# Optimization experiments

Hardware: AMD Instinct MI355X
Metric: run time of the kernel (lower is better)

## Reference

```python
import jax, jax.numpy as jnp
import numpy as np

C_IN = 3; IMG = 256; LAT = 256; K = 1024; L = 4
ENC = [128, 256, 512]; DEC = [512, 256, 128]


def conv2d(x, w, b, stride, pad):
    # x: NCHW, w: OIHW
    y = jax.lax.conv_general_dilated(x, w, (stride, stride), [(pad, pad), (pad, pad)],
                                     dimension_numbers=('NCHW', 'OIHW', 'NCHW'))
    return y + b[None, :, None, None]


def convT(x, w, b):
    # stride-2 transposed conv, kernel 4, 'SAME' -> doubles H,W. w: HWIO
    y = jax.lax.conv_transpose(x, w, (2, 2), 'SAME',
                               dimension_numbers=('NCHW', 'HWIO', 'NCHW'))
    return y + b[None, :, None, None]


def setup_inputs() -> dict:
    key = jax.random.key(0)
    ks = iter(jax.random.split(key, 32))
    def w(shape, fan_in):
        return jax.random.normal(next(ks), shape, jnp.float32) / np.float32(np.sqrt(fan_in))
    inp = {'x': jax.random.normal(next(ks), (8, C_IN, IMG, IMG), jnp.float32)}
    cin = C_IN
    for i, co in enumerate(ENC):
        inp[f'enc_w{i}'] = w((co, cin, 4, 4), cin * 16)
        inp[f'enc_b{i}'] = jnp.zeros((co,), jnp.float32)
        cin = co
    inp['proj_w'] = w((LAT, ENC[-1], 1, 1), ENC[-1])
    inp['proj_b'] = jnp.zeros((LAT,), jnp.float32)
    cin = LAT
    for i, co in enumerate(DEC):
        inp[f'dec_w{i}'] = w((4, 4, cin, co), cin * 16)
        inp[f'dec_b{i}'] = jnp.zeros((co,), jnp.float32)
        cin = co
    inp['out_w'] = w((C_IN, DEC[-1], 3, 3), DEC[-1] * 9)
    inp['out_b'] = jnp.zeros((C_IN,), jnp.float32)
    # per-level codebooks, uniform(-1/K, 1/K) as in the torch init
    inp['emb'] = jax.random.uniform(next(ks), (L, K, LAT), jnp.float32, -1.0 / K, 1.0 / K)
    return inp


def reference(x, enc_w0, enc_b0, enc_w1, enc_b1, enc_w2, enc_b2,
              proj_w, proj_b, dec_w0, dec_b0, dec_w1, dec_b1, dec_w2, dec_b2,
              out_w, out_b, emb):
    # encoder: three stride-2 convs + ReLU
    h = x
    for w_, b_ in ((enc_w0, enc_b0), (enc_w1, enc_b1), (enc_w2, enc_b2)):
        h = jax.nn.relu(conv2d(h, w_, b_, 2, 1))
    z = conv2d(h, proj_w, proj_b, 1, 0)  # [B, LAT, 32, 32]

    # residual quantization over L levels
    B, C, H, W = z.shape
    r = z
    z_q = jnp.zeros_like(z)
    residuals, codes = [], []
    for l in range(L):
        E = emb[l]                                   # [K, C]
        rf = r.transpose(0, 2, 3, 1).reshape(-1, C)  # [B*H*W, C]
        # squared euclidean distance (argmin equal to cdist argmin)
        d2 = (jnp.sum(rf * rf, axis=1, keepdims=True)
              - 2.0 * (rf @ E.T)
              + jnp.sum(E * E, axis=1))
        idx = jnp.argmin(d2, axis=1)                 # [B*H*W]
        e = E[idx].reshape(B, H, W, C).transpose(0, 3, 1, 2)
        residuals.append(r)
        codes.append(idx.reshape(B, H, W))
        z_q = z_q + e
        r = r - e

    # straight-through estimator
    z_q_st = z + jax.lax.stop_gradient(z_q - z)

    # decoder: three stride-2 transposed convs + ReLU, then 3x3 output conv
    d = z_q_st
    for w_, b_ in ((dec_w0, dec_b0), (dec_w1, dec_b1), (dec_w2, dec_b2)):
        d = jax.nn.relu(convT(d, w_, b_))
    recon = conv2d(d, out_w, out_b, 1, 1)  # [B, 3, 256, 256] == img_size, no interp
    return recon, z, z_q, jnp.stack(residuals), jnp.stack(codes)
```

## Files before the change

kernel.cpp:

```cpp
#include <hip/hip_runtime.h>
#include <hip/hip_bf16.h>
#include <cstdint>

#define BATCH 8
#define LATC 256
#define NCODE 1024
#define NLVL 4

typedef __attribute__((ext_vector_type(8))) short bf16x8v;
typedef __attribute__((ext_vector_type(4))) float f32x4v;

__device__ __forceinline__ unsigned short f2b(float f) {
  __hip_bfloat16 h = __float2bfloat16(f);
  return *reinterpret_cast<unsigned short*>(&h);
}

__device__ __forceinline__ void gl_lds16(const void* gptr, unsigned lds_byte_off) {
  unsigned m0v = __builtin_amdgcn_readfirstlane(lds_byte_off);
  asm volatile("s_mov_b32 m0, %0\n"
               "global_load_lds_dwordx4 %1, off\n" ::"s"(m0v), "v"(gptr)
               : "memory");
}

template <int CIN, int COUT, int HIN, int CI_CHUNK, int CO_TILE, int CI_SPLIT>
__global__ __launch_bounds__(256) void conv_enc2(
    const float* __restrict__ in, const float* __restrict__ w,
    const float* __restrict__ bias, float* __restrict__ out) {
  constexpr int WIN = HIN;
  constexpr int HOUT = HIN / 2, WOUT = WIN / 2;
  constexpr int PT1 = HOUT / 16;
  constexpr int NEL = CI_CHUNK * 34 * 34;
  constexpr int WUNITS = CI_CHUNK * CO_TILE * 4;
  constexpr int CIPS = CIN / CI_SPLIT;

  __shared__ float T[CI_CHUNK][34][40];
  __shared__ float4 Wsh[CI_CHUNK][CO_TILE][4];

  const int tid = threadIdx.x;
  const int lane = tid & 63;
  const int wv = __builtin_amdgcn_readfirstlane(tid >> 6);
  const int cog = lane >> 5;
  const int pxi = lane & 31;
  const int m = pxi >> 2;
  const int ox4 = pxi & 3;
  const int co_loc0 = (wv * 2 + cog) * 8;

  const int bx = blockIdx.x;
  const int n = bx / (PT1 * PT1);
  const int pt = bx % (PT1 * PT1);
  const int oh0 = (pt / PT1) * 16, ow0 = (pt % PT1) * 16;
  const int hbase = 2 * oh0 - 1, wbase = 2 * ow0 - 1;
  const int co_blk = blockIdx.y * CO_TILE;
  const int split = (CI_SPLIT > 1) ? blockIdx.z : 0;
  const int ci_base = split * CIPS;

  float acc[2][4][2][4];
#pragma unroll
  for (int cl = 0; cl < 2; ++cl)
#pragma unroll
    for (int j = 0; j < 4; ++j) {
      float b = (CI_SPLIT == 1 || split == 0) ? bias[co_blk + co_loc0 + cl * 4 + j] : 0.f;
#pragma unroll
      for (int dy = 0; dy < 2; ++dy)
#pragma unroll
        for (int dx = 0; dx < 4; ++dx) acc[cl][j][dy][dx] = b;
    }

  for (int ch = ci_base; ch < ci_base + CIPS; ch += CI_CHUNK) {
    for (int u = tid; u < NEL; u += 256) {
      int cir = u / 1156;
      int rem = u - cir * 1156;
      int r = rem / 34, c = rem - r * 34;
      int hi = hbase + r, wi = wbase + c;
      float v = 0.f;
      if ((unsigned)hi < (unsigned)HIN && (unsigned)wi < (unsigned)WIN)
        v = in[((long long)(n * CIN + ch + cir) * HIN + hi) * WIN + wi];
      T[cir][r][(((r >> 2) & 1) << 2) + c] = v;
    }
    for (int u = tid; u < WUNITS; u += 256) {
      int k4 = u & 3;
      int rem = u >> 2;
      int co = rem % CO_TILE, ci = rem / CO_TILE;
      Wsh[ci][co][k4] =
          *(const float4*)&w[((long long)(co_blk + co) * CIN + ch + ci) * 16 + k4 * 4];
    }
    __syncthreads();
#pragma unroll
    for (int cir = 0; cir < CI_CHUNK; ++cir) {
      float xv[6][10];
#pragma unroll
      for (int roff = 0; roff < 6; ++roff) {
        int row = 4 * m + roff;
        const float* base = &T[cir][row][(((row >> 2) & 1) << 2) + 8 * ox4];
        float4 qa = *(const float4*)base;
        float4 qb = *(const float4*)(base + 4);
        float4 qc = *(const float4*)(base + 8);
        xv[roff][0] = qa.x; xv[roff][1] = qa.y; xv[roff][2] = qa.z; xv[roff][3] = qa.w;
        xv[roff][4] = qb.x; xv[roff][5] = qb.y; xv[roff][6] = qb.z; xv[roff][7] = qb.w;
        xv[roff][8] = qc.x; xv[roff][9] = qc.y;
      }
#pragma unroll
      for (int cl = 0; cl < 2; ++cl)
#pragma unroll
        for (int j = 0; j < 4; ++j) {
          int co_l = co_loc0 + cl * 4 + j;
#pragma unroll
          for (int kh = 0; kh < 4; ++kh) {
            float4 wq = Wsh[cir][co_l][kh];
            float wt0 = wq.x, wt1 = wq.y, wt2 = wq.z, wt3 = wq.w;
#pragma unroll
            for (int dy = 0; dy < 2; ++dy) {
              int r = 2 * dy + kh;
#pragma unroll
              for (int dx = 0; dx < 4; ++dx) {
                acc[cl][j][dy][dx] = fmaf(xv[r][2 * dx + 0], wt0, acc[cl][j][dy][dx]);
                acc[cl][j][dy][dx] = fmaf(xv[r][2 * dx + 1], wt1, acc[cl][j][dy][dx]);
                acc[cl][j][dy][dx] = fmaf(xv[r][2 * dx + 2], wt2, acc[cl][j][dy][dx]);
                acc[cl][j][dy][dx] = fmaf(xv[r][2 * dx + 3], wt3, acc[cl][j][dy][dx]);
              }
            }
          }
        }
    }
    __syncthreads();
  }
  const long long psz = (long long)BATCH * COUT * HOUT * WOUT;
  float* __restrict__ ob_ptr = out + (CI_SPLIT > 1 ? (long long)split * psz : 0LL);
#pragma unroll
  for (int cl = 0; cl < 2; ++cl)
#pragma unroll
    for (int j = 0; j < 4; ++j) {
      int co = co_blk + co_loc0 + cl * 4 + j;
#pragma unroll
      for (int dy = 0; dy < 2; ++dy) {
        int oh = oh0 + 2 * m + dy, ow = ow0 + 4 * ox4;
        float4 v;
#pragma unroll
        for (int dx = 0; dx < 4; ++dx) {
          float t = acc[cl][j][dy][dx];
          if (CI_SPLIT == 1) t = fmaxf(t, 0.f);
          ((float*)&v)[dx] = t;
        }
        *reinterpret_cast<float4*>(
            &ob_ptr[((long long)(n * COUT + co) * HOUT + oh) * WOUT + ow]) = v;
      }
    }
}

template <int S, bool RELU>
__global__ __launch_bounds__(256) void fuse_sum(const float* __restrict__ p,
                                                float* __restrict__ out, long long n4) {
  long long i = (long long)blockIdx.x * 256 + threadIdx.x;
  long long stride = (long long)gridDim.x * 256;
  long long N = n4 * 4;
  for (; i < n4; i += stride) {
    float4 a = *(const float4*)&p[i * 4];
#pragma unroll
    for (int s = 1; s < S; ++s) {
      float4 b = *(const float4*)&p[(long long)s * N + i * 4];
      a.x += b.x; a.y += b.y; a.z += b.z; a.w += b.w;
    }
    if (RELU) {
      a.x = fmaxf(a.x, 0.f); a.y = fmaxf(a.y, 0.f);
      a.z = fmaxf(a.z, 0.f); a.w = fmaxf(a.w, 0.f);
    }
    *(float4*)&out[i * 4] = a;
  }
}

__global__ __launch_bounds__(256) void wtrans(const float* __restrict__ pw,
                                              float* __restrict__ pwT) {
  int gid = blockIdx.x * 256 + threadIdx.x;
  if (gid >= 512 * 256) return;
  int ci = gid >> 8, co = gid & 255;
  pwT[gid] = pw[co * 512 + ci];
}

template <int CI_SPLIT>
__global__ __launch_bounds__(256) void conv1x1_v2(
    const float* __restrict__ in, const float* __restrict__ pwT,
    const float* __restrict__ bias, float* __restrict__ out) {
  constexpr int CIPS = 512 / CI_SPLIT;
  __shared__ float Tx[16][128];
  const int tid = threadIdx.x;
  const int lane = tid & 63;
  const int wv = __builtin_amdgcn_readfirstlane(tid >> 6);
  const int p0 = lane * 2;
  const int bx = blockIdx.x;
  const int n = bx >> 3, pxb = bx & 7;
  const int px_base = pxb * 128;
  const int co_base = blockIdx.y * 64 + wv * 16;
  const int split = (CI_SPLIT > 1) ? blockIdx.z : 0;
  const int ci0 = split * CIPS;

  float acc[4][4][2];
#pragma unroll
  for (int cl = 0; cl < 4; ++cl)
#pragma unroll
    for (int j = 0; j < 4; ++j) {
      float b = (CI_SPLIT == 1 || split == 0) ? bias[co_base + cl * 4 + j] : 0.f;
      acc[cl][j][0] = b; acc[cl][j][1] = b;
    }

  for (int ch = ci0; ch < ci0 + CIPS; ch += 16) {
    for (int u = tid; u < 2048; u += 256) {
      int cir = u >> 7, p = u & 127;
      Tx[cir][p] = in[(long long)(n * 512 + ch + cir) * 1024 + px_base + p];
    }
    __syncthreads();
#pragma unroll
    for (int cir = 0; cir < 16; ++cir) {
      float2 xv = *reinterpret_cast<const float2*>(&Tx[cir][p0]);
#pragma unroll
      for (int cl = 0; cl < 4; ++cl) {
        const float* __restrict__ wp = pwT + (ch + cir) * 256 + co_base + cl * 4;
#pragma unroll
        for (int j = 0; j < 4; ++j) {
          float wt = wp[j];
          acc[cl][j][0] = fmaf(xv.x, wt, acc[cl][j][0]);
          acc[cl][j][1] = fmaf(xv.y, wt, acc[cl][j][1]);
        }
      }
    }
    __syncthreads();
  }
  const long long psz = (long long)BATCH * 256 * 1024;
  float* __restrict__ ob = out + (CI_SPLIT > 1 ? (long long)split * psz : 0LL);
#pragma unroll
  for (int cl = 0; cl < 4; ++cl)
#pragma unroll
    for (int j = 0; j < 4; ++j) {
      int co = co_base + cl * 4 + j;
      *reinterpret_cast<float2*>(&ob[(long long)(n * 256 + co) * 1024 + px_base + p0]) =
          make_float2(acc[cl][j][0], acc[cl][j][1]);
    }
}

__global__ __launch_bounds__(256) void emb_norms(
    const float* __restrict__ emb, float* __restrict__ en) {
  int k = blockIdx.x * blockDim.x + threadIdx.x;
  if (k >= NLVL * NCODE) return;
  const float* __restrict__ e = emb + (long long)k * LATC;
  float s = 0.f;
  for (int c = 0; c < LATC; ++c) s = fmaf(e[c], e[c], s);
  en[k] = s;
}

#define RQ_P 32
#define RQ_CT 32
#define RQ_RS 260

__global__ __launch_bounds__(256) void rq_kernel2(
    const float* __restrict__ z, const float* __restrict__ emb,
    const float* __restrict__ en, float* __restrict__ zq_out,
    float* __restrict__ resid_out, float* __restrict__ codes_out) {
  __shared__ float e_sh[RQ_CT * RQ_RS];
  __shared__ float r_sh[RQ_P * RQ_RS];
  __shared__ float sum_sh[RQ_P];
  __shared__ int code_sh[RQ_P];
  const int tid = threadIdx.x;
  const int blk = blockIdx.x;
  const int n = (blk * RQ_P) >> 10;
  const int hw0 = (blk * RQ_P) & 1023;
  const long long zb = ((long long)n * LATC) * 1024 + hw0;

  for (int it = 0; it < 32; ++it) {
    int u = it * 256 + tid;
    int c = u >> 5, pix = u & 31;
    float v = z[zb + (long long)c * 1024 + pix];
    r_sh[pix * RQ_RS + c] = v;
    resid_out[((long long)n * LATC + c) * 1024 + hw0 + pix] = v;
  }
  __syncthreads();

  const int code_l = tid & 31;
  const int pixoff = tid >> 5;
  const int upix = tid >> 3;
  const int ucg = tid & 7;

  for (int l = 0; l < NLVL; ++l) {
    {
      float s = 0.f;
#pragma unroll
      for (int it = 0; it < 8; ++it) {
        int c4 = ucg + it * 8;
        float4 r4 = *(const float4*)&r_sh[upix * RQ_RS + c4 * 4];
        s += r4.x * r4.x + r4.y * r4.y + r4.z * r4.z + r4.w * r4.w;
      }
      s += __shfl_xor(s, 1); s += __shfl_xor(s, 2); s += __shfl_xor(s, 4);
      if (ucg == 0) sum_sh[upix] = s;
    }
    __syncthreads();
    const float* __restrict__ E = emb + (long long)l * NCODE * LATC;
    const float* __restrict__ enl = en + l * NCODE;
    float best[4]; int bidx[4];
#pragma unroll
    for (int g = 0; g < 4; ++g) { best[g] = 3.4e38f; bidx[g] = 0; }
    for (int tile = 0; tile < NCODE / RQ_CT; ++tile) {
      const float* __restrict__ Et = E + (long long)tile * RQ_CT * LATC;
      for (int it = 0; it < 32; ++it) {
        int u = it * 256 + tid;
        int cc = u >> 8, ch = u & 255;
        e_sh[cc * RQ_RS + ch] = Et[cc * LATC + ch];
      }
      __syncthreads();
      float acc[4] = {0.f, 0.f, 0.f, 0.f};
      for (int c4 = 0; c4 < 64; ++c4) {
        float4 e4 = *(const float4*)&e_sh[code_l * RQ_RS + c4 * 4];
#pragma unroll
        for (int g = 0; g < 4; ++g) {
          float4 r4 = *(const float4*)&r_sh[(g * 8 + pixoff) * RQ_RS + c4 * 4];
          acc[g] = fmaf(r4.x, e4.x, acc[g]);
          acc[g] = fmaf(r4.y, e4.y, acc[g]);
          acc[g] = fmaf(r4.z, e4.z, acc[g]);
          acc[g] = fmaf(r4.w, e4.w, acc[g]);
        }
      }
      int code = tile * RQ_CT + code_l;
      float ek2 = enl[code];
#pragma unroll
      for (int g = 0; g < 4; ++g) {
        float d2 = (sum_sh[g * 8 + pixoff] - 2.f * acc[g]) + ek2;
        if (d2 < best[g]) { best[g] = d2; bidx[g] = code; }
      }
      __syncthreads();
    }
#pragma unroll
    for (int g = 0; g < 4; ++g) {
      float bd = best[g]; int bi = bidx[g];
#pragma unroll
      for (int m = 1; m < 32; m <<= 1) {
        float od = __shfl_xor(bd, m);
        int oi = __shfl_xor(bi, m);
        if (od < bd || (od == bd && oi < bi)) { bd = od; bi = oi; }
      }
      if (code_l == 0) {
        int pix = g * 8 + pixoff;
        code_sh[pix] = bi;
        codes_out[(long long)(l * BATCH + n) * 1024 + hw0 + pix] = (float)bi;
      }
    }
    __syncthreads();
    {
      int sel = code_sh[upix];
      const float* __restrict__ esel = E + (long long)sel * LATC;
#pragma unroll
      for (int it = 0; it < 8; ++it) {
        int c4 = ucg + it * 8;
        float4 r4 = *(const float4*)&r_sh[upix * RQ_RS + c4 * 4];
        float4 e4 = *(const float4*)&esel[c4 * 4];
        r4.x -= e4.x; r4.y -= e4.y; r4.z -= e4.z; r4.w -= e4.w;
        *(float4*)&r_sh[upix * RQ_RS + c4 * 4] = r4;
        if (l < NLVL - 1) {
          long long rb = ((long long)((l + 1) * BATCH + n) * LATC + c4 * 4) * 1024 + hw0 + upix;
          resid_out[rb] = r4.x;
          resid_out[rb + 1024] = r4.y;
          resid_out[rb + 2048] = r4.z;
          resid_out[rb + 3072] = r4.w;
        }
      }
    }
    __syncthreads();
  }
  for (int it = 0; it < 32; ++it) {
    int u = it * 256 + tid;
    int c = u >> 5, pix = u & 31;
    float zv = z[zb + (long long)c * 1024 + pix];
    zq_out[zb + (long long)c * 1024 + pix] = zv - r_sh[pix * RQ_RS + c];
  }
}

__global__ __launch_bounds__(256) void to_nhwc_s1(const float* __restrict__ zq,
                                                  unsigned short* __restrict__ o) {
  __shared__ float tsh[32][33];
  int bx = blockIdx.x;
  int ct = bx & 7, y = (bx >> 3) & 31, n = bx >> 8;
  int tid = threadIdx.x;
  int x = tid & 31, cl = tid >> 5;
#pragma unroll
  for (int it = 0; it < 4; ++it) {
    int ci = it * 8 + cl;
    tsh[ci][x] = zq[((long long)(n * 256 + ct * 32 + ci) * 32 + y) * 32 + x];
  }
  __syncthreads();
  int ci = tid & 31, xg = tid >> 5;
#pragma unroll
  for (int it = 0; it < 4; ++it) {
    int xw = it * 8 + xg;
    o[(((long long)n * 34 + y + 1) * 34 + xw + 1) * 256 + ct * 32 + ci] = f2b(tsh[ci][xw]);
  }
}

__global__ __launch_bounds__(256) void wprep_k(const float* __restrict__ w,
                                               unsigned short* __restrict__ o,
                                               int CINc, int COUTc) {
  long long total = 16LL * CINc * COUTc;
  long long gid = (long long)blockIdx.x * 256 + threadIdx.x;
  if (gid >= total) return;
  int ci32 = (int)(gid & 31); long long t = gid >> 5;
  int co = (int)(t % COUTc); t /= COUTc;
  int tap = (int)(t & 3); t >>= 2;
  int nch = CINc / 32;
  int ch = (int)(t % nch); int phase = (int)(t / nch);
  int py = phase >> 1, px = phase & 1;
  int ky = py + 2 * (tap >> 1), kx = px + 2 * (tap & 1);
  int ci = ch * 32 + ci32;
  float v = w[(((long long)ky * 4 + kx) * CINc + ci) * COUTc + co];
  o[gid] = f2b(v);
}

template <int CIN, int COUT, int TH, int TW, int Hi, int Wi, bool OUT_NCHW>
__global__ __launch_bounds__(256) void convt2(
    const unsigned short* __restrict__ xin, const unsigned short* __restrict__ wprep,
    const float* __restrict__ bias, unsigned short* __restrict__ outp) {
  constexpr int TWP = TW + 2, ROWS = TH + 2;
  constexpr int Hp = Hi + 2, Wp = Wi + 2;
  constexpr int NCH = CIN / 32;
  constexpr int XUNITS = ROWS * TWP;
  constexpr int XPAD = ((XUNITS + 255) / 256) * 256;
  constexpr int WBASE = 4 * XPAD;
  __shared__ unsigned short lds[(4 * XPAD + 4 * 256) * 8];

  const int tid = threadIdx.x;
  const int wv = tid >> 6, lane = tid & 63;
  const int l15 = lane & 15, seg = lane >> 4;

  constexpr int SW = Wi / TW, SH = Hi / TH;
  const int bx = blockIdx.x;
  const int n = bx / (SH * SW);
  const int srem = bx % (SH * SW);
  const int i0 = (srem / SW) * TH, j0 = (srem % SW) * TW;
  const int cob0 = blockIdx.y * 64;
  const int phase = blockIdx.z;
  const int pyp = phase >> 1, pxp = phase & 1;

  const unsigned short* xsrc = xin + (long long)n * Hp * Wp * CIN;

  f32x4v acc[4][4];
  if (!OUT_NCHW) {
#pragma unroll
    for (int b = 0; b < 4; ++b) {
      float bv = bias[cob0 + b * 16 + l15];
      f32x4v v = {bv, bv, bv, bv};
#pragma unroll
      for (int a = 0; a < 4; ++a) acc[a][b] = v;
    }
  } else {
#pragma unroll
    for (int a = 0; a < 4; ++a) {
      f32x4v v;
#pragma unroll
      for (int q = 0; q < 4; ++q) v[q] = bias[cob0 + a * 16 + seg * 4 + q];
#pragma unroll
      for (int b = 0; b < 4; ++b) acc[a][b] = v;
    }
  }

  for (int ch = 0; ch < NCH; ++ch) {
    __syncthreads();
#pragma unroll
    for (int sg = 0; sg < 4; ++sg) {
#pragma unroll
      for (int it = 0; it < XPAD / 256; ++it) {
        int u = it * 256 + tid;
        int us = u < XUNITS ? u : XUNITS - 1;
        int row = us / TWP, col = us % TWP;
        const unsigned short* g =
            xsrc + ((long long)(i0 + row) * Wp + (j0 + col)) * CIN + ch * 32 + sg * 8;
        gl_lds16(g, (unsigned)(unsigned long long)(const void*)&lds[(sg * XPAD + u) * 8]);
      }
    }
    {
      const unsigned short* wb = wprep + ((long long)phase * NCH + ch) * 4 * COUT * 32;
      int tap = tid >> 6, co = tid & 63;
#pragma unroll
      for (int sg = 0; sg < 4; ++sg) {
        const unsigned short* g = wb + ((long long)tap * COUT + cob0 + co) * 32 + sg * 8;
        gl_lds16(g, (unsigned)(unsigned long long)(const void*)&lds[(WBASE + sg * 256 + tid) * 8]);
      }
    }
    asm volatile("s_waitcnt vmcnt(0)" ::: "memory");
    __syncthreads();
#pragma unroll
    for (int t = 0; t < 4; ++t) {
      int oy = (t >> 1) - 1 + pyp, ox = (t & 1) - 1 + pxp;
      bf16x8v xf[4], wf[4];
#pragma unroll
      for (int i = 0; i < 4; ++i) {
        int p = wv * 64 + i * 16 + l15;
        int r = p / TW, c = p % TW;
        int xrow = r + oy + 1, xcol = c + ox + 1;
        xf[i] = *(const bf16x8v*)&lds[(seg * XPAD + xrow * TWP + xcol) * 8];
        wf[i] = *(const bf16x8v*)&lds[(WBASE + seg * 256 + t * 64 + i * 16 + l15) * 8];
      }
#pragma unroll
      for (int a = 0; a < 4; ++a)
#pragma unroll
        for (int b = 0; b < 4; ++b) {
          if (OUT_NCHW)
            acc[a][b] = __builtin_amdgcn_mfma_f32_16x16x32_bf16(wf[a], xf[b], acc[a][b], 0, 0, 0);
          else
            acc[a][b] = __builtin_amdgcn_mfma_f32_16x16x32_bf16(xf[a], wf[b], acc[a][b], 0, 0, 0);
        }
    }
  }

  if (!OUT_NCHW) {
    constexpr int Wpo = 2 * Wi + 2;
    long long ob_n = (long long)n * (2 * Hi + 2) * Wpo * COUT;
#pragma unroll
    for (int a = 0; a < 4; ++a)
#pragma unroll
      for (int q = 0; q < 4; ++q) {
        int p = wv * 64 + a * 16 + seg * 4 + q;
        int r = p / TW, c = p % TW;
        int yo = 2 * (i0 + r) + pyp + 1, xo = 2 * (j0 + c) + pxp + 1;
        long long ob = ob_n + ((long long)yo * Wpo + xo) * COUT + cob0;
#pragma unroll
        for (int b = 0; b < 4; ++b) {
          float v = fmaxf(acc[a][b][q], 0.f);
          outp[ob + b * 16 + l15] = f2b(v);
        }
      }
  } else {
    constexpr int Ho = 2 * Hi, Wo = 2 * Wi;
#pragma unroll
    for (int a = 0; a < 4; ++a)
#pragma unroll
      for (int q = 0; q < 4; ++q) {
        int co = cob0 + a * 16 + seg * 4 + q;
#pragma unroll
        for (int b = 0; b < 4; ++b) {
          int p = wv * 64 + b * 16 + l15;
          int r = p / TW, c = p % TW;
          int yo = 2 * (i0 + r) + pyp, xo = 2 * (j0 + c) + pxp;
          float v = fmaxf(acc[a][b][q], 0.f);
          outp[((long long)(n * COUT + co) * Ho + yo) * Wo + xo] = f2b(v);
        }
      }
  }
}

__global__ __launch_bounds__(256) void conv3x3_v2(
    const __hip_bfloat16* __restrict__ in, const float* __restrict__ w,
    const float* __restrict__ bias, float* __restrict__ out) {
  constexpr int H = 256, W = 256, CIN = 128;
  __shared__ float Wsh[3 * CIN * 9];
  __shared__ float T[4][34][35];

  const int tid = threadIdx.x;
  for (int u = tid; u < 3 * CIN * 9; u += 256) Wsh[u] = w[u];

  const int bx = blockIdx.x;
  const int n = bx >> 6;
  const int t8 = bx & 63;
  const int y0 = (t8 >> 3) * 32, x0 = (t8 & 7) * 32;
  const int ty = (tid >> 4) * 2;
  const int tx = (tid & 15) * 2;

  float acc[3][2][2];
#pragma unroll
  for (int co = 0; co < 3; ++co) {
    float b = bias[co];
    acc[co][0][0] = b; acc[co][0][1] = b; acc[co][1][0] = b; acc[co][1][1] = b;
  }

  for (int ch = 0; ch < CIN; ch += 4) {
    __syncthreads();
    for (int u = tid; u < 4 * 34 * 34; u += 256) {
      int ci = u / (34 * 34);
      int rem = u % (34 * 34);
      int r = rem / 34, c = rem % 34;
      int yy = y0 + r - 1, xx = x0 + c - 1;
      float v = 0.f;
      if ((unsigned)yy < (unsigned)H && (unsigned)xx < (unsigned)W)
        v = __bfloat162float(in[((long long)(n * CIN + ch + ci) * H + yy) * W + xx]);
      T[ci][r][c] = v;
    }
    __syncthreads();
#pragma unroll
    for (int ci = 0; ci < 4; ++ci) {
      float xv[4][4];
#pragma unroll
      for (int r = 0; r < 4; ++r)
#pragma unroll
        for (int c = 0; c < 4; ++c) xv[r][c] = T[ci][ty + r][tx + c];
#pragma unroll
      for (int co = 0; co < 3; ++co) {
        const float* __restrict__ wp = &Wsh[(co * CIN + ch + ci) * 9];
#pragma unroll
        for (int kh = 0; kh < 3; ++kh)
#pragma unroll
          for (int kw = 0; kw < 3; ++kw) {
            float wt = wp[kh * 3 + kw];
            acc[co][0][0] = fmaf(xv[kh][kw], wt, acc[co][0][0]);
            acc[co][0][1] = fmaf(xv[kh][kw + 1], wt, acc[co][0][1]);
            acc[co][1][0] = fmaf(xv[kh + 1][kw], wt, acc[co][1][0]);
            acc[co][1][1] = fmaf(xv[kh + 1][kw + 1], wt, acc[co][1][1]);
          }
      }
    }
  }
#pragma unroll
  for (int co = 0; co < 3; ++co)
#pragma unroll
    for (int dy = 0; dy < 2; ++dy) {
      long long ob = ((long long)(n * 3 + co) * H + y0 + ty + dy) * W + x0 + tx;
      *reinterpret_cast<float2*>(&out[ob]) = make_float2(acc[co][dy][0], acc[co][dy][1]);
    }
}

extern "C" void kernel_launch(void* const* d_in, const int* in_sizes, int n_in,
                              void* d_out, int out_size, void* d_ws, size_t ws_size,
                              hipStream_t stream) {
  const float* x   = (const float*)d_in[0];
  const float* ew0 = (const float*)d_in[1];  const float* eb0 = (const float*)d_in[2];
  const float* ew1 = (const float*)d_in[3];  const float* eb1 = (const float*)d_in[4];
  const float* ew2 = (const float*)d_in[5];  const float* eb2 = (const float*)d_in[6];
  const float* pw  = (const float*)d_in[7];  const float* pb  = (const float*)d_in[8];
  const float* dw0 = (const float*)d_in[9];  const float* db0 = (const float*)d_in[10];
  const float* dw1 = (const float*)d_in[11]; const float* db1 = (const float*)d_in[12];
  const float* dw2 = (const float*)d_in[13]; const float* db2 = (const float*)d_in[14];
  const float* ow  = (const float*)d_in[15]; const float* ob  = (const float*)d_in[16];
  const float* emb = (const float*)d_in[17];

  float* out   = (float*)d_out;
  float* recon = out;
  float* z     = out + 1572864;
  float* zq    = out + 3670016;
  float* resid = out + 5767168;
  float* codes = out + 14155776;

  char* ws = (char*)d_ws;
  dim3 blk(256);
  auto g = [](long long tot) { return dim3((unsigned)((tot + 255) / 256)); };

  const size_t OFF_S1IN  = 0ULL;
  const size_t OFF_S1OUT = 4734976ULL;
  const size_t OFF_WP1   = 40419328ULL;
  const size_t OFF_WP2   = 44613632ULL;
  const size_t OFF_P     = 67108864ULL;
  const size_t OFF_E2    = 134217728ULL;
  const size_t OFF_PWT   = 150994944ULL;
  const size_t OFF_DD2   = 0ULL;
  const size_t OFF_S2OUT = 134217728ULL;
  const size_t OFF_WP3   = 203440128ULL;
  const size_t OFF_EN    = 204488704ULL;
  const size_t WS_NEED   = 204505088ULL;

  if (ws_size < WS_NEED) return;

  float* e0  = (float*)(ws);
  float* p2  = (float*)(ws + OFF_P);
  float* e1  = (float*)(ws);
  float* p3  = (float*)(ws + OFF_P);
  float* e2  = (float*)(ws + OFF_E2);
  float* q1  = (float*)(ws + OFF_P);
  float* en  = (float*)(ws + OFF_EN);
  float* pwT = (float*)(ws + OFF_PWT);
  unsigned short* s1in  = (unsigned short*)(ws + OFF_S1IN);
  unsigned short* s1out = (unsigned short*)(ws + OFF_S1OUT);
  unsigned short* s2out = (unsigned short*)(ws + OFF_S2OUT);
  unsigned short* dd2   = (unsigned short*)(ws + OFF_DD2);
  unsigned short* wp1   = (unsigned short*)(ws + OFF_WP1);
  unsigned short* wp2   = (unsigned short*)(ws + OFF_WP2);
  unsigned short* wp3   = (unsigned short*)(ws + OFF_WP3);

  emb_norms<<<g(4096), blk, 0, stream>>>(emb, en);

  conv_enc2<3, 128, 256, 3, 64, 1><<<dim3(512, 2, 1), blk, 0, stream>>>(x, ew0, eb0, e0);
  conv_enc2<128, 256, 128, 4, 64, 4><<<dim3(128, 4, 4), blk, 0, stream>>>(e0, ew1, eb1, p2);
  fuse_sum<4, true><<<dim3(4096), blk, 0, stream>>>(p2, e1, 8388608 / 4);
  conv_enc2<256, 512, 64, 4, 64, 4><<<dim3(32, 8, 4), blk, 0, stream>>>(e1, ew2, eb2, p3);
  fuse_sum<4, true><<<dim3(2048), blk, 0, stream>>>(p3, e2, 4194304 / 4);
  wtrans<<<g(512 * 256), blk, 0, stream>>>(pw, pwT);
  conv1x1_v2<4><<<dim3(64, 4, 4), blk, 0, stream>>>(e2, pwT, pb, q1);
  fuse_sum<4, false><<<dim3(1024), blk, 0, stream>>>(q1, z, 2097152 / 4);

  rq_kernel2<<<dim3(256), blk, 0, stream>>>(z, emb, en, zq, resid, codes);

  hipMemsetAsync(ws + OFF_S1IN, 0, 4734976ULL, stream);
  hipMemsetAsync(ws + OFF_S1OUT, 0, 35684352ULL, stream);
  hipMemsetAsync(ws + OFF_S2OUT, 0, 69222400ULL, stream);
  to_nhwc_s1<<<dim3(2048), blk, 0, stream>>>(zq, s1in);
  wprep_k<<<g(16LL * 256 * 512), blk, 0, stream>>>(dw0, wp1, 256, 512);
  wprep_k<<<g(16LL * 512 * 256), blk, 0, stream>>>(dw1, wp2, 512, 256);
  wprep_k<<<g(16LL * 256 * 128), blk, 0, stream>>>(dw2, wp3, 256, 128);

  convt2<256, 512, 8, 32, 32, 32, false>
      <<<dim3(32, 8, 4), dim3(256), 0, stream>>>(s1in, wp1, db0, s1out);
  convt2<512, 256, 4, 64, 64, 64, false>
      <<<dim3(128, 4, 4), dim3(256), 0, stream>>>(s1out, wp2, db1, s2out);
  convt2<256, 128, 4, 64, 128, 128, true>
      <<<dim3(512, 2, 4), dim3(256), 0, stream>>>(s2out, wp3, db2, dd2);

  conv3x3_v2<<<dim3(512), blk, 0, stream>>>((const __hip_bfloat16*)dd2, ow, ob, recon);
}
```

Before: 2.777 ms.

## Restructure residual quantization with register-tiled 4x4 codes-by-pixels dot products

The RQ kernel now keeps the residual transposed in LDS (channel-major) and gives each thread a 4-code by 4-pixel register tile. Each wave owns a quarter of the codebook, and codebook rows are read directly from global memory instead of being staged through LDS tiles with per-tile barriers. A cross-wave argmin reduction through shared memory replaces the per-tile shuffle reduction. This aims to raise arithmetic intensity and remove barrier and LDS staging overhead, at the cost of strided uncached-looking global reads of the codebook and more registers.

```diff
diff --git a/kernel.cpp b/kernel.cpp
--- a/kernel.cpp
+++ b/kernel.cpp
@@ -246,35 +246,35 @@
   en[k] = s;
 }
 
-#define RQ_P 32
-#define RQ_CT 32
-#define RQ_RS 260
-
-__global__ __launch_bounds__(256) void rq_kernel2(
+__global__ __launch_bounds__(256) void rq_kernel3(
     const float* __restrict__ z, const float* __restrict__ emb,
     const float* __restrict__ en, float* __restrict__ zq_out,
     float* __restrict__ resid_out, float* __restrict__ codes_out) {
-  __shared__ float e_sh[RQ_CT * RQ_RS];
-  __shared__ float r_sh[RQ_P * RQ_RS];
-  __shared__ float sum_sh[RQ_P];
-  __shared__ int code_sh[RQ_P];
+  __shared__ float rT[256 * 32];
+  __shared__ float sum_sh[32];
+  __shared__ float red_d[4][32];
+  __shared__ int red_i[4][32];
+  __shared__ int code_sh[32];
+
   const int tid = threadIdx.x;
+  const int lane = tid & 63;
+  const int w = __builtin_amdgcn_readfirstlane(tid >> 6);
+  const int cs = lane & 7;
+  const int ps = lane >> 3;
   const int blk = blockIdx.x;
-  const int n = (blk * RQ_P) >> 10;
-  const int hw0 = (blk * RQ_P) & 1023;
+  const int n = (blk * 32) >> 10;
+  const int hw0 = (blk * 32) & 1023;
   const long long zb = ((long long)n * LATC) * 1024 + hw0;
 
   for (int it = 0; it < 32; ++it) {
     int u = it * 256 + tid;
     int c = u >> 5, pix = u & 31;
     float v = z[zb + (long long)c * 1024 + pix];
-    r_sh[pix * RQ_RS + c] = v;
+    rT[c * 32 + pix] = v;
     resid_out[((long long)n * LATC + c) * 1024 + hw0 + pix] = v;
   }
   __syncthreads();
 
-  const int code_l = tid & 31;
-  const int pixoff = tid >> 5;
   const int upix = tid >> 3;
   const int ucg = tid & 7;
 
@@ -284,79 +284,116 @@
 #pragma unroll
       for (int it = 0; it < 8; ++it) {
         int c4 = ucg + it * 8;
-        float4 r4 = *(const float4*)&r_sh[upix * RQ_RS + c4 * 4];
-        s += r4.x * r4.x + r4.y * r4.y + r4.z * r4.z + r4.w * r4.w;
+        float x = rT[(c4 * 4 + 0) * 32 + upix];
+        float y = rT[(c4 * 4 + 1) * 32 + upix];
+        float zz = rT[(c4 * 4 + 2) * 32 + upix];
+        float ww = rT[(c4 * 4 + 3) * 32 + upix];
+        s += x * x + y * y + zz * zz + ww * ww;
       }
       s += __shfl_xor(s, 1); s += __shfl_xor(s, 2); s += __shfl_xor(s, 4);
       if (ucg == 0) sum_sh[upix] = s;
     }
     __syncthreads();
+
     const float* __restrict__ E = emb + (long long)l * NCODE * LATC;
     const float* __restrict__ enl = en + l * NCODE;
-    float best[4]; int bidx[4];
-#pragma unroll
-    for (int g = 0; g < 4; ++g) { best[g] = 3.4e38f; bidx[g] = 0; }
-    for (int tile = 0; tile < NCODE / RQ_CT; ++tile) {
-      const float* __restrict__ Et = E + (long long)tile * RQ_CT * LATC;
-      for (int it = 0; it < 32; ++it) {
-        int u = it * 256 + tid;
-        int cc = u >> 8, ch = u & 255;
-        e_sh[cc * RQ_RS + ch] = Et[cc * LATC + ch];
-      }
-      __syncthreads();
-      float acc[4] = {0.f, 0.f, 0.f, 0.f};
+    float bd[4]; int bi[4];
+#pragma unroll
+    for (int i = 0; i < 4; ++i) { bd[i] = 3.4e38f; bi[i] = 0; }
+
+    for (int pass = 0; pass < 8; ++pass) {
+      const int cbase = w * 256 + pass * 32 + cs * 4;
+      float acc[4][4];
+#pragma unroll
+      for (int j = 0; j < 4; ++j)
+#pragma unroll
+        for (int i = 0; i < 4; ++i) acc[j][i] = 0.f;
+#pragma unroll 4
       for (int c4 = 0; c4 < 64; ++c4) {
-        float4 e4 = *(const float4*)&e_sh[code_l * RQ_RS + c4 * 4];
-#pragma unroll
-        for (int g = 0; g < 4; ++g) {
-          float4 r4 = *(const float4*)&r_sh[(g * 8 + pixoff) * RQ_RS + c4 * 4];
-          acc[g] = fmaf(r4.x, e4.x, acc[g]);
-          acc[g] = fmaf(r4.y, e4.y, acc[g]);
-          acc[g] = fmaf(r4.z, e4.z, acc[g]);
-          acc[g] = fmaf(r4.w, e4.w, acc[g]);
-        }
-      }
-      int code = tile * RQ_CT + code_l;
-      float ek2 = enl[code];
-#pragma unroll
-      for (int g = 0; g < 4; ++g) {
-        float d2 = (sum_sh[g * 8 + pixoff] - 2.f * acc[g]) + ek2;
-        if (d2 < best[g]) { best[g] = d2; bidx[g] = code; }
-      }
-      __syncthreads();
-    }
-#pragma unroll
-    for (int g = 0; g < 4; ++g) {
-      float bd = best[g]; int bi = bidx[g];
-#pragma unroll
-      for (int m = 1; m < 32; m <<= 1) {
-        float od = __shfl_xor(bd, m);
-        int oi = __shfl_xor(bi, m);
-        if (od < bd || (od == bd && oi < bi)) { bd = od; bi = oi; }
-      }
-      if (code_l == 0) {
-        int pix = g * 8 + pixoff;
-        code_sh[pix] = bi;
-        codes_out[(long long)(l * BATCH + n) * 1024 + hw0 + pix] = (float)bi;
-      }
-    }
-    __syncthreads();
+        float4 ee[4];
+#pragma unroll
+        for (int j = 0; j < 4; ++j)
+          ee[j] = *(const float4*)&E[(long long)(cbase + j) * LATC + c4 * 4];
+        float4 rr[4];
+#pragma unroll
+        for (int s = 0; s < 4; ++s)
+          rr[s] = *(const float4*)&rT[(c4 * 4 + s) * 32 + ps * 4];
+#pragma unroll
+        for (int j = 0; j < 4; ++j) {
+          acc[j][0] = fmaf(ee[j].x, rr[0].x, acc[j][0]);
+          acc[j][0] = fmaf(ee[j].y, rr[1].x, acc[j][0]);
+          acc[j][0] = fmaf(ee[j].z, rr[2].x, acc[j][0]);
+          acc[j][0] = fmaf(ee[j].w, rr[3].x, acc[j][0]);
+          acc[j][1] = fmaf(ee[j].x, rr[0].y, acc[j][1]);
+          acc[j][1] = fmaf(ee[j].y, rr[1].y, acc[j][1]);
+          acc[j][1] = fmaf(ee[j].z, rr[2].y, acc[j][1]);
+          acc[j][1] = fmaf(ee[j].w, rr[3].y, acc[j][1]);
+          acc[j][2] = fmaf(ee[j].x, rr[0].z, acc[j][2]);
+          acc[j][2] = fmaf(ee[j].y, rr[1].z, acc[j][2]);
+          acc[j][2] = fmaf(ee[j].z, rr[2].z, acc[j][2]);
+          acc[j][2] = fmaf(ee[j].w, rr[3].z, acc[j][2]);
+          acc[j][3] = fmaf(ee[j].x, rr[0].w, acc[j][3]);
+          acc[j][3] = fmaf(ee[j].y, rr[1].w, acc[j][3]);
+          acc[j][3] = fmaf(ee[j].z, rr[2].w, acc[j][3]);
+          acc[j][3] = fmaf(ee[j].w, rr[3].w, acc[j][3]);
+        }
+      }
+#pragma unroll
+      for (int j = 0; j < 4; ++j) {
+        float ek2 = enl[cbase + j];
+#pragma unroll
+        for (int i = 0; i < 4; ++i) {
+          float d2 = (sum_sh[ps * 4 + i] - 2.f * acc[j][i]) + ek2;
+          if (d2 < bd[i]) { bd[i] = d2; bi[i] = cbase + j; }
+        }
+      }
+    }
+
+#pragma unroll
+    for (int i = 0; i < 4; ++i) {
+      float d = bd[i]; int ix = bi[i];
+#pragma unroll
+      for (int mm = 1; mm < 8; mm <<= 1) {
+        float od = __shfl_xor(d, mm);
+        int oi = __shfl_xor(ix, mm);
+        if (od < d || (od == d && oi < ix)) { d = od; ix = oi; }
+      }
+      if (cs == 0) { red_d[w][ps * 4 + i] = d; red_i[w][ps * 4 + i] = ix; }
+    }
+    __syncthreads();
+    if (tid < 32) {
+      float d = red_d[0][tid]; int ix = red_i[0][tid];
+#pragma unroll
+      for (int ww = 1; ww < 4; ++ww) {
+        float od = red_d[ww][tid]; int oi = red_i[ww][tid];
+        if (od < d || (od == d && oi < ix)) { d = od; ix = oi; }
+      }
+      code_sh[tid] = ix;
+      codes_out[(long long)(l * BATCH + n) * 1024 + hw0 + tid] = (float)ix;
+    }
+    __syncthreads();
+
     {
       int sel = code_sh[upix];
       const float* __restrict__ esel = E + (long long)sel * LATC;
 #pragma unroll
       for (int it = 0; it < 8; ++it) {
         int c4 = ucg + it * 8;
-        float4 r4 = *(const float4*)&r_sh[upix * RQ_RS + c4 * 4];
         float4 e4 = *(const float4*)&esel[c4 * 4];
-        r4.x -= e4.x; r4.y -= e4.y; r4.z -= e4.z; r4.w -= e4.w;
-        *(float4*)&r_sh[upix * RQ_RS + c4 * 4] = r4;
+        float r0 = rT[(c4 * 4 + 0) * 32 + upix] - e4.x;
+        float r1 = rT[(c4 * 4 + 1) * 32 + upix] - e4.y;
+        float r2 = rT[(c4 * 4 + 2) * 32 + upix] - e4.z;
+        float r3 = rT[(c4 * 4 + 3) * 32 + upix] - e4.w;
+        rT[(c4 * 4 + 0) * 32 + upix] = r0;
+        rT[(c4 * 4 + 1) * 32 + upix] = r1;
+        rT[(c4 * 4 + 2) * 32 + upix] = r2;
+        rT[(c4 * 4 + 3) * 32 + upix] = r3;
         if (l < NLVL - 1) {
           long long rb = ((long long)((l + 1) * BATCH + n) * LATC + c4 * 4) * 1024 + hw0 + upix;
-          resid_out[rb] = r4.x;
-          resid_out[rb + 1024] = r4.y;
-          resid_out[rb + 2048] = r4.z;
-          resid_out[rb + 3072] = r4.w;
+          resid_out[rb] = r0;
+          resid_out[rb + 1024] = r1;
+          resid_out[rb + 2048] = r2;
+          resid_out[rb + 3072] = r3;
         }
       }
     }
@@ -366,7 +403,7 @@
     int u = it * 256 + tid;
     int c = u >> 5, pix = u & 31;
     float zv = z[zb + (long long)c * 1024 + pix];
-    zq_out[zb + (long long)c * 1024 + pix] = zv - r_sh[pix * RQ_RS + c];
+    zq_out[zb + (long long)c * 1024 + pix] = zv - rT[c * 32 + pix];
   }
 }
 
@@ -677,7 +714,7 @@
   conv1x1_v2<4><<<dim3(64, 4, 4), blk, 0, stream>>>(e2, pwT, pb, q1);
   fuse_sum<4, false><<<dim3(1024), blk, 0, stream>>>(q1, z, 2097152 / 4);
 
-  rq_kernel2<<<dim3(256), blk, 0, stream>>>(z, emb, en, zq, resid, codes);
+  rq_kernel3<<<dim3(256), blk, 0, stream>>>(z, emb, en, zq, resid, codes);
 
   hipMemsetAsync(ws + OFF_S1IN, 0, 4734976ULL, stream);
   hipMemsetAsync(ws + OFF_S1OUT, 0, 35684352ULL, stream);
```

Result: slower. 3.112 ms (+12.1%).
